# Kernel tuning notes

Hardware: AMD Instinct MI355X
Metric: run time of the kernel (lower is better)

## Reference

```python
import jax, jax.numpy as jnp
import numpy as np
from jax import lax

N_BLOCKS = 5
POOL = 15
N_HEADS = 8
LATENT = 32
N_EXPERTS = 4


def setup_inputs() -> dict:
    key = jax.random.key(0)
    ks = jax.random.split(key, 24)
    B, T, D = 4, 2048, 512
    H = 2 * D  # expert_dim
    s = 0.02
    f = lambda k, shp: (jax.random.normal(k, shp, jnp.float32) * s)
    return {
        'x': jax.random.normal(ks[0], (B, T, D), jnp.float32),
        # TemporalGating gate_proj
        'tg_w': f(ks[1], (D, N_BLOCKS)), 'tg_b': jnp.zeros((N_BLOCKS,), jnp.float32),
        # DualScaleFusion
        'mp_w': f(ks[2], (D, D)), 'mp_b': jnp.zeros((D,), jnp.float32),
        'fu_w': f(ks[3], (2 * D, D)), 'fu_b': jnp.zeros((D,), jnp.float32),
        # MLAAttention (all no-bias)
        'wc': f(ks[4], (D, LATENT)), 'wk': f(ks[5], (LATENT, D)),
        'wv': f(ks[6], (LATENT, D)), 'wq': f(ks[7], (D, D)), 'wo': f(ks[8], (D, D)),
        # RMSNorms
        's1': jnp.ones((D,), jnp.float32), 's2': jnp.ones((D,), jnp.float32),
        # GatedMoE
        'wr': f(ks[9], (D, N_EXPERTS)), 'br': jnp.zeros((N_EXPERTS,), jnp.float32),
        'wg': f(ks[10], (D, D)), 'bg': jnp.zeros((D,), jnp.float32),
        'w1': f(ks[11], (N_EXPERTS, D, H)), 'b1': jnp.zeros((N_EXPERTS, H), jnp.float32),
        'w2': f(ks[12], (N_EXPERTS, H, D)), 'b2': jnp.zeros((N_EXPERTS, D), jnp.float32),
    }


def _temporal_gate(x, tg_w, tg_b):
    B, T, D = x.shape
    bs = T // N_BLOCKS
    tl = N_BLOCKS * bs
    r = x[:, :tl].reshape(B, N_BLOCKS, bs, D)          # [B,nb,bs,D]
    bm = r.mean(axis=2)                                 # [B,nb,D]
    imp = jax.nn.softmax(bm @ tg_w + tg_b, axis=-1)     # [B,nb,nb]
    imp = imp.mean(axis=-1, keepdims=True)              # [B,nb,1]
    g = (r * imp[..., None]).reshape(B, tl, D)
    return jnp.pad(g, ((0, 0), (0, T - tl), (0, 0)))


def _dual_scale(x, mp_w, mp_b, fu_w, fu_b):
    # AveragePooling1D(pool=15, stride=1, SAME): TF excludes padding from the mean.
    B, T, D = x.shape
    sums = lax.reduce_window(x, 0.0, lax.add, (1, POOL, 1), (1, 1, 1), 'SAME')
    cnt = lax.reduce_window(jnp.ones((1, T, 1), x.dtype), 0.0, lax.add,
                            (1, POOL, 1), (1, 1, 1), 'SAME')
    macro = sums / cnt
    macro_feat = macro @ mp_w + mp_b
    return jnp.concatenate([x, macro_feat], axis=-1) @ fu_w + fu_b


def _mla_attn(x, wc, wk, wv, wq, wo):
    B, T, D = x.shape
    dh = D // N_HEADS
    split = lambda t: t.reshape(B, T, N_HEADS, dh).transpose(0, 2, 1, 3)
    latent = x @ wc                                      # [B,T,L]
    K, V, Q = split(latent @ wk), split(latent @ wv), split(x @ wq)
    scores = jnp.einsum('bhqd,bhkd->bhqk', Q, K) / jnp.sqrt(jnp.float32(dh))
    causal = jnp.tril(jnp.ones((T, T), jnp.float32))
    scores = scores + (1.0 - causal) * -1e9
    attn = jax.nn.softmax(scores, axis=-1)
    out = jnp.einsum('bhqk,bhkd->bhqd', attn, V).transpose(0, 2, 1, 3).reshape(B, T, D)
    return out @ wo


def _rmsnorm(x, scale, eps=1e-6):
    var = jnp.mean(jnp.square(x), axis=-1, keepdims=True)
    return scale * (x * lax.rsqrt(var + eps))


def _moe(x, wr, br, wg, bg, w1, b1, w2, b2):
    w = jax.nn.softmax(x @ wr + br, axis=-1)             # [B,T,E]
    xg = x * jax.nn.sigmoid(x @ wg + bg)
    h = jax.nn.gelu(jnp.einsum('btd,edh->bteh', xg, w1) + b1, approximate=False)
    eo = jnp.einsum('bteh,ehd->bted', h, w2) + b2        # [B,T,E,D]
    return jnp.einsum('bted,bte->btd', eo, w)


def reference(x, tg_w, tg_b, mp_w, mp_b, fu_w, fu_b, wc, wk, wv, wq, wo,
              s1, s2, wr, br, wg, bg, w1, b1, w2, b2):
    xf = _temporal_gate(x, tg_w, tg_b)
    xfu = _dual_scale(xf, mp_w, mp_b, fu_w, fu_b)
    x1 = _rmsnorm(x + _mla_attn(xfu, wc, wk, wv, wq, wo), s1)
    return _rmsnorm(x1 + _moe(x1, wr, br, wg, bg, w1, b1, w2, b2), s2)
```

## Files before the change

kernel.cpp:

```cpp
#include <hip/hip_runtime.h>
#include <math.h>

#define B_   4
#define T_   2048
#define D_   512
#define TOK  (B_*T_)
#define TL_  2045
#define GATE 0.2f

typedef unsigned short u16;
typedef __attribute__((ext_vector_type(8))) short short8;
typedef __attribute__((ext_vector_type(4))) float f32x4;

static __device__ __forceinline__ u16 f2u(float f){
    union { float f; unsigned u; } a; a.f = f;
    unsigned r = a.u + 0x7fffu + ((a.u >> 16) & 1u);
    return (u16)(r >> 16);
}
static __device__ __forceinline__ float u2f(u16 u){
    union { unsigned u; float f; } a; a.u = ((unsigned)u) << 16;
    return a.f;
}
static __device__ __forceinline__ f32x4 mfma16(short8 a, short8 b, f32x4 c){
    return __builtin_amdgcn_mfma_f32_16x16x32_bf16(a, b, c, 0, 0, 0);
}
static __device__ __forceinline__ void glds16(const u16* g, u16* l){
    __builtin_amdgcn_global_load_lds((const __attribute__((address_space(1))) void*)g,
                                     (__attribute__((address_space(3))) void*)l, 16, 0, 0);
}

__global__ __launch_bounds__(256) void gatepool_kernel(
    const float* __restrict__ x, u16* __restrict__ xfcat)
{
    int idx = blockIdx.x*256 + threadIdx.x;
    int d = idx & 511, g = idx >> 9;
    int b = g >> 7, t0 = (g & 127) << 4;
    const float* xp = x + ((size_t)b*2048)*512 + d;
    float v[30];
    #pragma unroll
    for (int j = 0; j < 30; ++j){
        int u = t0 - 7 + j;
        v[j] = (u >= 0 && u < TL_) ? xp[(size_t)u*512] : 0.f;
    }
    float p[31]; p[0] = 0.f;
    #pragma unroll
    for (int j = 0; j < 30; ++j) p[j+1] = p[j] + v[j];
    u16* xc = xfcat + ((size_t)(b*2048 + t0))*1024 + d;
    #pragma unroll
    for (int i = 0; i < 16; ++i){
        int t = t0 + i;
        float sum = p[i+15] - p[i];
        int lo = t-7; if (lo < 0) lo = 0;
        int hi = t+7; if (hi > 2047) hi = 2047;
        xc[(size_t)i*1024]       = f2u((t < TL_) ? GATE*v[i+7] : 0.f);
        xc[(size_t)i*1024 + 512] = f2u(GATE * sum / (float)(hi - lo + 1));
    }
}

struct TJob { const float* src; u16* dst; int K, N, ldout, coloff, tiles; float scale; };
struct TJobs { TJob j[12]; int n; };

__global__ __launch_bounds__(256) void tconv_all_kernel(TJobs JJ){
    __shared__ float t[32][33];
    int idx = blockIdx.x;
    int jb = 0;
    while (jb < JJ.n - 1 && idx >= JJ.j[jb].tiles){ idx -= JJ.j[jb].tiles; ++jb; }
    TJob J = JJ.j[jb];
    int tX = J.N >> 5;
    int k0 = (idx / tX) * 32, n0 = (idx % tX) * 32;
    int tx = threadIdx.x & 31, ty = threadIdx.x >> 5;
    #pragma unroll
    for (int i = 0; i < 32; i += 8)
        t[ty+i][tx] = J.src[(size_t)(k0+ty+i)*J.N + n0+tx];
    __syncthreads();
    #pragma unroll
    for (int i = 0; i < 32; i += 8)
        J.dst[(size_t)(n0+ty+i)*J.ldout + J.coloff + k0+tx] = f2u(J.scale * t[tx][ty+i]);
}

__global__ void convert_kernel(const float* __restrict__ in, u16* __restrict__ out){
    int idx = blockIdx.x*256 + threadIdx.x;
    out[idx] = f2u(in[idx]);
}

__global__ __launch_bounds__(256) void biasfold_kernel(
    const float* __restrict__ fu_b, const float* __restrict__ mp_b,
    const float* __restrict__ fu_w, float* __restrict__ out)
{
    int n = blockIdx.x, tid = threadIdx.x;
    float s = mp_b[tid]*fu_w[(size_t)(512+tid)*512 + n]
            + mp_b[tid+256]*fu_w[(size_t)(768+tid)*512 + n];
    for (int off = 32; off; off >>= 1) s += __shfl_down(s, off);
    __shared__ float ws[4];
    if ((tid & 63) == 0) ws[tid >> 6] = s;
    __syncthreads();
    if (tid == 0) out[n] = fu_b[n] + ws[0]+ws[1]+ws[2]+ws[3];
}

__global__ __launch_bounds__(256) void sgemm_kernel(const float* __restrict__ A,
    const float* __restrict__ B, u16* __restrict__ dstT, int ldT, int K){
    __shared__ float As[16][65];
    __shared__ float Bs[16][65];
    int tid = threadIdx.x;
    int tx = tid & 15, ty = tid >> 4;
    int m0 = blockIdx.y*64, n0 = blockIdx.x*64;
    int arow = tid >> 2, akq = (tid & 3) * 4;
    int bk = tid >> 4, bn = (tid & 15) * 4;
    float acc[4][4] = {};
    for (int k0 = 0; k0 < K; k0 += 16){
        const float* Ap = A + (size_t)(m0+arow)*K + k0 + akq;
        As[akq+0][arow]=Ap[0]; As[akq+1][arow]=Ap[1];
        As[akq+2][arow]=Ap[2]; As[akq+3][arow]=Ap[3];
        const float* Bp = B + (size_t)(k0+bk)*512 + n0 + bn;
        Bs[bk][bn+0]=Bp[0]; Bs[bk][bn+1]=Bp[1];
        Bs[bk][bn+2]=Bp[2]; Bs[bk][bn+3]=Bp[3];
        __syncthreads();
        #pragma unroll
        for (int kk = 0; kk < 16; ++kk){
            float av[4], bv[4];
            #pragma unroll
            for (int i=0;i<4;++i) av[i]=As[kk][ty*4+i];
            #pragma unroll
            for (int j=0;j<4;++j) bv[j]=Bs[kk][tx*4+j];
            #pragma unroll
            for (int i=0;i<4;++i)
                #pragma unroll
                for (int j=0;j<4;++j) acc[i][j] += av[i]*bv[j];
        }
        __syncthreads();
    }
    #pragma unroll
    for (int i=0;i<4;++i)
        #pragma unroll
        for (int j=0;j<4;++j)
            dstT[(size_t)(n0+tx*4+j)*ldT + m0+ty*4+i] = f2u(acc[i][j]);
}

#define GF_GELU   1
#define GF_ACCUM  2
#define GF_RSCOL  4
#define GF_GLU    8
#define GF_F32OUT 16
#define GF_TRANS  32

template<int MT>
__global__ __launch_bounds__(256) void mgemm_kernel(
    const u16* __restrict__ A, int lda, const u16* __restrict__ Bt, int ldb,
    const float* __restrict__ bias, const float* __restrict__ rs,
    const u16* __restrict__ glu, void* __restrict__ Cp, int ldc,
    int K, int flags)
{
    constexpr int MI = MT/32;
    __shared__ u16 As[MT*64];
    __shared__ u16 Bs[128*64];
    int tid = threadIdx.x;
    int wave = tid >> 6, lane = tid & 63;
    int n16 = lane & 15, quad = lane >> 4;
    int m0 = blockIdx.y * MT, n0 = blockIdx.x * 128;
    int wr = (wave >> 1) * (MT/2), wc = (wave & 1) * 64;

    f32x4 acc[MI][4] = {};

    for (int k0 = 0; k0 < K; k0 += 64){
        #pragma unroll
        for (int i = 0; i < MT/32; ++i){
            int s = i*256 + tid;
            int row = s >> 3, g = (s & 7) ^ (row & 7);
            glds16(A + (size_t)(m0+row)*lda + k0 + g*8, As + (size_t)s*8);
        }
        #pragma unroll
        for (int i = 0; i < 4; ++i){
            int s = i*256 + tid;
            int row = s >> 3, g = (s & 7) ^ (row & 7);
            glds16(Bt + (size_t)(n0+row)*ldb + k0 + g*8, Bs + (size_t)s*8);
        }
        __syncthreads();
        #pragma unroll
        for (int ks = 0; ks < 2; ++ks){
            short8 af[MI], bf[4];
            #pragma unroll
            for (int mi = 0; mi < MI; ++mi){
                int row = wr + mi*16 + n16;
                int g = (ks*4 + quad) ^ (row & 7);
                af[mi] = *(const short8*)&As[row*64 + g*8];
            }
            #pragma unroll
            for (int ni = 0; ni < 4; ++ni){
                int row = wc + ni*16 + n16;
                int g = (ks*4 + quad) ^ (row & 7);
                bf[ni] = *(const short8*)&Bs[row*64 + g*8];
            }
            #pragma unroll
            for (int mi = 0; mi < MI; ++mi)
                #pragma unroll
                for (int ni = 0; ni < 4; ++ni)
                    acc[mi][ni] = mfma16(af[mi], bf[ni], acc[mi][ni]);
        }
        __syncthreads();
    }

    if (flags & GF_TRANS){
        #pragma unroll
        for (int mi = 0; mi < MI; ++mi){
            int row0 = m0 + wr + mi*16 + quad*4;
            #pragma unroll
            for (int ni = 0; ni < 4; ++ni){
                int col = n0 + wc + ni*16 + n16;
                ushort4 h4;
                h4.x = f2u(acc[mi][ni][0]); h4.y = f2u(acc[mi][ni][1]);
                h4.z = f2u(acc[mi][ni][2]); h4.w = f2u(acc[mi][ni][3]);
                *(ushort4*)&((u16*)Cp)[(size_t)col*ldc + row0] = h4;
            }
        }
        return;
    }

    #pragma unroll
    for (int mi = 0; mi < MI; ++mi){
        #pragma unroll
        for (int reg = 0; reg < 4; ++reg){
            int row = m0 + wr + mi*16 + quad*4 + reg;
            #pragma unroll
            for (int ni = 0; ni < 4; ++ni){
                int col = n0 + wc + ni*16 + n16;
                float v = acc[mi][ni][reg];
                if (bias) v += bias[col];
                if (flags & GF_GELU)  v = 0.5f*v*(1.f + erff(v*0.70710678118f));
                if (flags & GF_GLU)   v = u2f(glu[(size_t)row*512 + col]) / (1.f + __expf(-v));
                if (flags & GF_RSCOL) v *= rs[(size_t)row*4 + (col >> 10)];
                size_t ci = (size_t)row*ldc + col;
                if (flags & GF_ACCUM)       ((float*)Cp)[ci] += v;
                else if (flags & GF_F32OUT) ((float*)Cp)[ci]  = v;
                else                        ((u16*)Cp)[ci]    = f2u(v);
            }
        }
    }
}

__global__ __launch_bounds__(256) void flash_kernel(
    const u16* __restrict__ QK,
    const u16* __restrict__ VT,
    u16* __restrict__ O)
{
    int bid = blockIdx.x;
    int qt = 15 - (bid >> 5);
    int bh = bid & 31;
    int h = bh & 7, b = bh >> 3;
    __shared__ u16 Ks[64*64];
    __shared__ u16 Vt[64*64];
    __shared__ u16 Ps[4][32*64];
    int tid = threadIdx.x;
    int wave = tid >> 6, lane = tid & 63;
    int n16 = lane & 15, quad = lane >> 4;
    size_t btok = (size_t)b*2048;
    size_t tok0 = btok + qt*128;
    int rowbase[2];
    rowbase[0] = qt*128 + wave*32;
    rowbase[1] = rowbase[0] + 16;

    short8 aq[2][2];
    #pragma unroll
    for (int mi = 0; mi < 2; ++mi)
        #pragma unroll
        for (int ks = 0; ks < 2; ++ks)
            aq[mi][ks] = *(const short8*)&QK[(tok0 + wave*32 + mi*16 + n16)*1024
                                            + h*64 + ks*32 + quad*8];

    float m_st[2][4], l_st[2][4];
    #pragma unroll
    for (int mi = 0; mi < 2; ++mi)
        #pragma unroll
        for (int r = 0; r < 4; ++r){ m_st[mi][r] = -3.0e38f; l_st[mi][r] = 0.f; }
    f32x4 ov[2][4] = {};

    int nkt = 2*qt + 2;
    for (int kt = 0; kt < nkt; ++kt){
        __syncthreads();
        {
            int r = tid >> 2;
            int g0 = (tid & 3) * 2;
            const uint4* kp = (const uint4*)&QK[(btok + kt*64 + r)*1024 + 512 + h*64 + g0*8];
            uint4 ka = kp[0], kb = kp[1];
            *(uint4*)&Ks[r*64 + ((g0  ) ^ (r&7))*8] = ka;
            *(uint4*)&Ks[r*64 + ((g0+1) ^ (r&7))*8] = kb;
            const uint4* vp = (const uint4*)&VT[(size_t)(h*64 + r)*8192 + btok + kt*64 + g0*8];
            uint4 va = vp[0], vb = vp[1];
            *(uint4*)&Vt[r*64 + ((g0  ) ^ (r&7))*8] = va;
            *(uint4*)&Vt[r*64 + ((g0+1) ^ (r&7))*8] = vb;
        }
        __syncthreads();

        #pragma unroll
        for (int mi = 0; mi < 2; ++mi){
            if (kt*64 > rowbase[mi] + 15) continue;
            f32x4 s[4];
            #pragma unroll
            for (int ct = 0; ct < 4; ++ct){
                f32x4 a = {};
                #pragma unroll
                for (int ks = 0; ks < 2; ++ks){
                    short8 bk = *(const short8*)&Ks[(ct*16+n16)*64 + (((ks*4+quad) ^ (n16&7))*8)];
                    a = mfma16(aq[mi][ks], bk, a);
                }
                s[ct] = a;
            }
            if (kt*64 + 63 > rowbase[mi]){
                #pragma unroll
                for (int ct = 0; ct < 4; ++ct){
                    int col = kt*64 + ct*16 + n16;
                    #pragma unroll
                    for (int r = 0; r < 4; ++r)
                        if (col > rowbase[mi] + quad*4 + r) s[ct][r] = -3.0e38f;
                }
            }
            #pragma unroll
            for (int r = 0; r < 4; ++r){
                float mx = fmaxf(fmaxf(s[0][r], s[1][r]), fmaxf(s[2][r], s[3][r]));
                #pragma unroll
                for (int off = 1; off < 16; off <<= 1) mx = fmaxf(mx, __shfl_xor(mx, off));
                float mn = fmaxf(m_st[mi][r], mx);
                float al = __expf(m_st[mi][r] - mn);
                m_st[mi][r] = mn;
                float sum = 0.f;
                #pragma unroll
                for (int ct = 0; ct < 4; ++ct){
                    float p = __expf(s[ct][r] - mn);
                    s[ct][r] = p; sum += p;
                }
                #pragma unroll
                for (int off = 1; off < 16; off <<= 1) sum += __shfl_xor(sum, off);
                l_st[mi][r] = l_st[mi][r]*al + sum;
                #pragma unroll
                for (int dt = 0; dt < 4; ++dt) ov[mi][dt][r] *= al;
            }
            #pragma unroll
            for (int ct = 0; ct < 4; ++ct){
                int gg = ct*2 + (n16 >> 3);
                #pragma unroll
                for (int r = 0; r < 4; ++r){
                    int row = mi*16 + quad*4 + r;
                    Ps[wave][row*64 + ((gg ^ (row&7))*8) + (n16 & 7)] = f2u(s[ct][r]);
                }
            }
        }
        #pragma unroll
        for (int mi = 0; mi < 2; ++mi){
            if (kt*64 > rowbase[mi] + 15) continue;
            short8 ap[2];
            #pragma unroll
            for (int ks = 0; ks < 2; ++ks){
                int row = mi*16 + n16;
                ap[ks] = *(const short8*)&Ps[wave][row*64 + (((ks*4+quad) ^ (n16&7))*8)];
            }
            #pragma unroll
            for (int dt = 0; dt < 4; ++dt)
                #pragma unroll
                for (int ks = 0; ks < 2; ++ks){
                    short8 bv = *(const short8*)&Vt[(dt*16+n16)*64 + (((ks*4+quad) ^ (n16&7))*8)];
                    ov[mi][dt] = mfma16(ap[ks], bv, ov[mi][dt]);
                }
        }
    }
    #pragma unroll
    for (int mi = 0; mi < 2; ++mi)
        #pragma unroll
        for (int r = 0; r < 4; ++r){
            float inv = 1.f / l_st[mi][r];
            size_t row = tok0 + wave*32 + mi*16 + quad*4 + r;
            #pragma unroll
            for (int dt = 0; dt < 4; ++dt)
                O[row*512 + h*64 + dt*16 + n16] = f2u(ov[mi][dt][r] * inv);
        }
}

__global__ __launch_bounds__(256) void rmsnorm_kernel(
    const float* __restrict__ x, const u16* __restrict__ y,
    const float* __restrict__ scale, u16* __restrict__ out)
{
    int tok = blockIdx.x, tid = threadIdx.x;
    size_t base = (size_t)tok * 512;
    float v0 = x[base+tid]     + u2f(y[base+tid]);
    float v1 = x[base+tid+256] + u2f(y[base+tid+256]);
    float ss = v0*v0 + v1*v1;
    for (int off = 32; off; off >>= 1) ss += __shfl_down(ss, off);
    __shared__ float ws[4];
    if ((tid & 63) == 0) ws[tid >> 6] = ss;
    __syncthreads();
    float rstd = rsqrtf((ws[0]+ws[1]+ws[2]+ws[3])*(1.f/512.f) + 1e-6f);
    out[base+tid]     = f2u(scale[tid]     * v0 * rstd);
    out[base+tid+256] = f2u(scale[tid+256] * v1 * rstd);
}

__global__ __launch_bounds__(256) void final_kernel(
    const u16* __restrict__ x1, const float* __restrict__ moe,
    const float* __restrict__ rout, const float* __restrict__ b2,
    const float* __restrict__ scale, float* __restrict__ out)
{
    int tok = blockIdx.x, tid = threadIdx.x;
    size_t base = (size_t)tok * 512;
    float r0 = rout[tok*4+0], r1 = rout[tok*4+1], r2 = rout[tok*4+2], r3 = rout[tok*4+3];
    float bb0 = r0*b2[tid]     + r1*b2[512+tid]     + r2*b2[1024+tid]     + r3*b2[1536+tid];
    float bb1 = r0*b2[tid+256] + r1*b2[768+tid]     + r2*b2[1280+tid]     + r3*b2[1792+tid];
    float v0 = u2f(x1[base+tid])     + moe[base+tid]     + bb0;
    float v1 = u2f(x1[base+tid+256]) + moe[base+tid+256] + bb1;
    float ss = v0*v0 + v1*v1;
    for (int off = 32; off; off >>= 1) ss += __shfl_down(ss, off);
    __shared__ float ws[4];
    if ((tid & 63) == 0) ws[tid >> 6] = ss;
    __syncthreads();
    float rstd = rsqrtf((ws[0]+ws[1]+ws[2]+ws[3])*(1.f/512.f) + 1e-6f);
    out[base+tid]     = scale[tid]     * v0 * rstd;
    out[base+tid+256] = scale[tid+256] * v1 * rstd;
}

__global__ __launch_bounds__(256) void router_kernel(
    const u16* __restrict__ x1, const float* __restrict__ wr,
    const float* __restrict__ br, float* __restrict__ rout)
{
    int wid = threadIdx.x >> 6, lane = threadIdx.x & 63;
    int tok = blockIdx.x*4 + wid;
    const u16* xp = x1 + (size_t)tok*512;
    float p0=0.f, p1=0.f, p2=0.f, p3=0.f;
    for (int d = lane; d < 512; d += 64){
        float xv = u2f(xp[d]);
        p0 += xv*wr[d*4+0]; p1 += xv*wr[d*4+1];
        p2 += xv*wr[d*4+2]; p3 += xv*wr[d*4+3];
    }
    for (int off = 32; off; off >>= 1){
        p0 += __shfl_down(p0,off); p1 += __shfl_down(p1,off);
        p2 += __shfl_down(p2,off); p3 += __shfl_down(p3,off);
    }
    if (lane == 0){
        p0 += br[0]; p1 += br[1]; p2 += br[2]; p3 += br[3];
        float mx = fmaxf(fmaxf(p0,p1), fmaxf(p2,p3));
        float e0=__expf(p0-mx), e1=__expf(p1-mx), e2=__expf(p2-mx), e3=__expf(p3-mx);
        float inv = 1.f/(e0+e1+e2+e3);
        rout[tok*4+0]=e0*inv; rout[tok*4+1]=e1*inv;
        rout[tok*4+2]=e2*inv; rout[tok*4+3]=e3*inv;
    }
}

extern "C" void kernel_launch(void* const* d_in, const int* in_sizes, int n_in,
                              void* d_out, int out_size, void* d_ws, size_t ws_size,
                              hipStream_t stream)
{
    const float* x    = (const float*)d_in[0];
    const float* mp_w = (const float*)d_in[3];
    const float* mp_b = (const float*)d_in[4];
    const float* fu_w = (const float*)d_in[5];
    const float* fu_b = (const float*)d_in[6];
    const float* wc   = (const float*)d_in[7];
    const float* wk   = (const float*)d_in[8];
    const float* wv   = (const float*)d_in[9];
    const float* wq   = (const float*)d_in[10];
    const float* wo   = (const float*)d_in[11];
    const float* s1   = (const float*)d_in[12];
    const float* s2   = (const float*)d_in[13];
    const float* wr   = (const float*)d_in[14];
    const float* br   = (const float*)d_in[15];
    const float* wg   = (const float*)d_in[16];
    const float* bg   = (const float*)d_in[17];
    const float* w1   = (const float*)d_in[18];
    const float* b1   = (const float*)d_in[19];
    const float* w2   = (const float*)d_in[20];
    const float* b2   = (const float*)d_in[21];

    char* wsb = (char*)d_ws;
    const size_t MB = 1024*1024;
    u16*   wqkT   = (u16*)(wsb + 0);
    u16*   wcvT   = (u16*)(wsb + 1*MB);
    u16*   woT    = (u16*)(wsb + (3*MB)/2);
    u16*   wgT    = (u16*)(wsb + 2*MB);
    u16*   WfuT2  = (u16*)(wsb + (5*MB)/2);
    u16*   fuBT   = (u16*)(wsb + (7*MB)/2);
    u16*   mp_wB  = (u16*)(wsb + 4*MB);
    u16*   w1T    = (u16*)(wsb + (9*MB)/2);
    u16*   w2Ts   = (u16*)(wsb + (17*MB)/2);
    float* fubias = (float*)(wsb + (25*MB)/2);
    float* ROUT   = (float*)(wsb + (25*MB)/2 + 4096);
    u16*   XFcat = (u16*)(wsb + 13*MB);
    float* MOE   = (float*)(wsb + 13*MB);
    u16*   S3    = (u16*)(wsb + 13*MB);
    u16*   XFU   = (u16*)(wsb + 29*MB);
    u16*   XG    = (u16*)(wsb + 29*MB);
    u16*   QKb   = (u16*)(wsb + 37*MB);
    u16*   Hb    = (u16*)(wsb + 37*MB);
    u16*   VbT   = (u16*)(wsb + 53*MB);
    u16*   ATT   = (u16*)(wsb + 61*MB);
    u16*   x1h   = (u16*)(wsb + 69*MB);

    auto mg128 = [&](const u16* A, int lda, const u16* Bt, int ldb, const float* bias,
                     const float* rs, const u16* glu, void* C, int ldc,
                     int M, int N, int K, int flags){
        dim3 g(N/128, M/128);
        mgemm_kernel<128><<<g, 256, 0, stream>>>(A, lda, Bt, ldb, bias, rs, glu, C, ldc, K, flags);
    };
    auto mg64 = [&](const u16* A, int lda, const u16* Bt, int ldb, const float* bias,
                    const float* rs, const u16* glu, void* C, int ldc,
                    int M, int N, int K, int flags){
        dim3 g(N/128, M/64);
        mgemm_kernel<64><<<g, 256, 0, stream>>>(A, lda, Bt, ldb, bias, rs, glu, C, ldc, K, flags);
    };

    TJobs JJ;
    auto setj = [&](int i, const float* src, u16* dst, int K, int N, int ldout,
                    int coloff, float scale){
        JJ.j[i] = TJob{src, dst, K, N, ldout, coloff, (K/32)*(N/32), scale};
    };
    setj(0, wq,            wqkT,  512,  512,  512, 0, 0.125f);
    setj(1, wo,            woT,   512,  512,  512, 0, 1.f);
    setj(2, wg,            wgT,   512,  512,  512, 0, 1.f);
    setj(3, fu_w,          WfuT2, 512,  512, 1024, 0, 1.f);
    setj(4, fu_w + 512*512,fuBT,  512,  512,  512, 0, 1.f);
    int nt = 5*256;
    for (int e = 0; e < 4; ++e){
        setj(5+e, w1 + (size_t)e*512*1024, w1T + (size_t)e*1024*512, 512, 1024, 512, 0, 1.f);
        nt += 512;
    }
    JJ.n = 12;
    setj(9,  w2,                      w2Ts, 1024, 512, 4096, 0,    1.f);
    setj(10, w2 + (size_t)1*1024*512, w2Ts, 1024, 512, 4096, 1024, 1.f);
    setj(11, w2 + (size_t)2*1024*512, w2Ts, 1024, 512, 4096, 2048, 1.f);
    nt += 3*512;
    tconv_all_kernel<<<nt, 256, 0, stream>>>(JJ);
    TJobs J2; J2.n = 1;
    J2.j[0] = TJob{w2 + (size_t)3*1024*512, w2Ts, 1024, 512, 4096, 3072, 512, 1.f};
    tconv_all_kernel<<<512, 256, 0, stream>>>(J2);
    convert_kernel<<<512*512/256, 256, 0, stream>>>(mp_w, mp_wB);
    sgemm_kernel<<<dim3(8,8), 256, 0, stream>>>(wc, wk, wqkT + 512*512, 512, 32);
    sgemm_kernel<<<dim3(8,8), 256, 0, stream>>>(wc, wv, wcvT, 512, 32);
    biasfold_kernel<<<512, 256, 0, stream>>>(fu_b, mp_b, fu_w, fubias);
    mg64(fuBT, 512, mp_wB, 512, 0, 0, 0, WfuT2 + 512, 1024, 512, 512, 512, 0);

    gatepool_kernel<<<(TOK/16)*512/256, 256, 0, stream>>>(x, XFcat);
    mg64 (XFcat, 1024, WfuT2, 1024, fubias, 0, 0, XFU, 512, TOK, 512, 1024, 0);
    mg128(XFU, 512, wqkT, 512, 0, 0, 0, QKb, 1024, TOK, 1024, 512, 0);
    mg64 (XFU, 512, wcvT, 512, 0, 0, 0, VbT, 8192, TOK, 512, 512, GF_TRANS);
    flash_kernel<<<512, 256, 0, stream>>>(QKb, VbT, ATT);
    mg64 (ATT, 512, woT, 512, 0, 0, 0, S3, 512, TOK, 512, 512, 0);
    rmsnorm_kernel<<<TOK, 256, 0, stream>>>(x, S3, s1, x1h);
    router_kernel<<<TOK/4, 256, 0, stream>>>(x1h, wr, br, ROUT);
    mg64 (x1h, 512, wgT, 512, bg, 0, x1h, XG, 512, TOK, 512, 512, GF_GLU);
    for (int p = 0; p < 2; ++p){
        mg128(XG, 512, w1T + (size_t)p*2048*512, 512, b1 + p*2048, ROUT + p*2, 0,
              Hb, 2048, TOK, 2048, 512, GF_GELU | GF_RSCOL);
        mg64 (Hb, 2048, w2Ts + p*2048, 4096, 0, 0, 0,
              MOE, 512, TOK, 512, 2048, p ? GF_ACCUM : GF_F32OUT);
    }
    final_kernel<<<TOK, 256, 0, stream>>>(x1h, MOE, ROUT, b2, s2, (float*)d_out);
}
```

Before: 631.3 us.

## Fuse QK and V projections into one GEMM and restructure flash softmax

```diff
diff --git a/kernel.cpp b/kernel.cpp
--- a/kernel.cpp
+++ b/kernel.cpp
@@ -7,6 +7,7 @@
 #define TOK  (B_*T_)
 #define TL_  2045
 #define GATE 0.2f
+#define QSCALE 0.18033688011112043f
 
 typedef unsigned short u16;
 typedef __attribute__((ext_vector_type(8))) short short8;
@@ -58,7 +59,7 @@
 }
 
 struct TJob { const float* src; u16* dst; int K, N, ldout, coloff, tiles; float scale; };
-struct TJobs { TJob j[12]; int n; };
+struct TJobs { TJob j[13]; int n; };
 
 __global__ __launch_bounds__(256) void tconv_all_kernel(TJobs JJ){
     __shared__ float t[32][33];
@@ -98,7 +99,7 @@
 }
 
 __global__ __launch_bounds__(256) void sgemm_kernel(const float* __restrict__ A,
-    const float* __restrict__ B, u16* __restrict__ dstT, int ldT, int K){
+    const float* __restrict__ B, u16* __restrict__ dstT, float* __restrict__ outF, int K){
     __shared__ float As[16][65];
     __shared__ float Bs[16][65];
     int tid = threadIdx.x;
@@ -129,11 +130,19 @@
         }
         __syncthreads();
     }
-    #pragma unroll
-    for (int i=0;i<4;++i)
-        #pragma unroll
-        for (int j=0;j<4;++j)
-            dstT[(size_t)(n0+tx*4+j)*ldT + m0+ty*4+i] = f2u(acc[i][j]);
+    if (outF){
+        #pragma unroll
+        for (int i=0;i<4;++i)
+            #pragma unroll
+            for (int j=0;j<4;++j)
+                outF[(size_t)(m0+ty*4+i)*512 + n0+tx*4+j] = acc[i][j];
+    } else {
+        #pragma unroll
+        for (int i=0;i<4;++i)
+            #pragma unroll
+            for (int j=0;j<4;++j)
+                dstT[(size_t)(n0+tx*4+j)*512 + m0+ty*4+i] = f2u(acc[i][j]);
+    }
 }
 
 #define GF_GELU   1
@@ -141,14 +150,14 @@
 #define GF_RSCOL  4
 #define GF_GLU    8
 #define GF_F32OUT 16
-#define GF_TRANS  32
+#define GF_QKV    32
 
 template<int MT>
 __global__ __launch_bounds__(256) void mgemm_kernel(
     const u16* __restrict__ A, int lda, const u16* __restrict__ Bt, int ldb,
     const float* __restrict__ bias, const float* __restrict__ rs,
     const u16* __restrict__ glu, void* __restrict__ Cp, int ldc,
-    int K, int flags)
+    u16* __restrict__ Cp2, int K, int flags)
 {
     constexpr int MI = MT/32;
     __shared__ u16 As[MT*64];
@@ -199,17 +208,17 @@
         __syncthreads();
     }
 
-    if (flags & GF_TRANS){
+    if ((flags & GF_QKV) && n0 >= 1024){
         #pragma unroll
         for (int mi = 0; mi < MI; ++mi){
             int row0 = m0 + wr + mi*16 + quad*4;
             #pragma unroll
             for (int ni = 0; ni < 4; ++ni){
-                int col = n0 + wc + ni*16 + n16;
+                int col = n0 + wc + ni*16 + n16 - 1024;
                 ushort4 h4;
                 h4.x = f2u(acc[mi][ni][0]); h4.y = f2u(acc[mi][ni][1]);
                 h4.z = f2u(acc[mi][ni][2]); h4.w = f2u(acc[mi][ni][3]);
-                *(ushort4*)&((u16*)Cp)[(size_t)col*ldc + row0] = h4;
+                *(ushort4*)&Cp2[(size_t)col*8192 + row0] = h4;
             }
         }
         return;
@@ -254,23 +263,18 @@
     int n16 = lane & 15, quad = lane >> 4;
     size_t btok = (size_t)b*2048;
     size_t tok0 = btok + qt*128;
-    int rowbase[2];
-    rowbase[0] = qt*128 + wave*32;
-    rowbase[1] = rowbase[0] + 16;
-
-    short8 aq[2][2];
-    #pragma unroll
-    for (int mi = 0; mi < 2; ++mi)
+
+    short8 qf[2][2];
+    #pragma unroll
+    for (int g = 0; g < 2; ++g)
         #pragma unroll
         for (int ks = 0; ks < 2; ++ks)
-            aq[mi][ks] = *(const short8*)&QK[(tok0 + wave*32 + mi*16 + n16)*1024
-                                            + h*64 + ks*32 + quad*8];
-
-    float m_st[2][4], l_st[2][4];
-    #pragma unroll
-    for (int mi = 0; mi < 2; ++mi)
-        #pragma unroll
-        for (int r = 0; r < 4; ++r){ m_st[mi][r] = -3.0e38f; l_st[mi][r] = 0.f; }
+            qf[g][ks] = *(const short8*)&QK[(tok0 + wave*32 + g*16 + n16)*1024
+                                           + h*64 + ks*32 + quad*8];
+
+    int qlo[2];  qlo[0] = qt*128 + wave*32; qlo[1] = qlo[0] + 16;
+    int qrow[2]; qrow[0] = qlo[0] + n16;    qrow[1] = qlo[1] + n16;
+    float m_st[2] = {-3.0e38f, -3.0e38f}, l_st[2] = {0.f, 0.f};
     f32x4 ov[2][4] = {};
 
     int nkt = 2*qt + 2;
@@ -290,86 +294,94 @@
         }
         __syncthreads();
 
-        #pragma unroll
-        for (int mi = 0; mi < 2; ++mi){
-            if (kt*64 > rowbase[mi] + 15) continue;
-            f32x4 s[4];
+        bool act[2];
+        #pragma unroll
+        for (int g = 0; g < 2; ++g){
+            act[g] = (kt*64 <= qlo[g] + 15);
+            if (!act[g]) continue;
+            f32x4 st[4];
             #pragma unroll
             for (int ct = 0; ct < 4; ++ct){
                 f32x4 a = {};
                 #pragma unroll
                 for (int ks = 0; ks < 2; ++ks){
-                    short8 bk = *(const short8*)&Ks[(ct*16+n16)*64 + (((ks*4+quad) ^ (n16&7))*8)];
-                    a = mfma16(aq[mi][ks], bk, a);
+                    short8 kf = *(const short8*)&Ks[(ct*16+n16)*64 + (((ks*4+quad) ^ (n16&7))*8)];
+                    a = mfma16(kf, qf[g][ks], a);
                 }
-                s[ct] = a;
-            }
-            if (kt*64 + 63 > rowbase[mi]){
+                st[ct] = a;
+            }
+            if (kt*64 + 63 > qlo[g]){
                 #pragma unroll
                 for (int ct = 0; ct < 4; ++ct){
-                    int col = kt*64 + ct*16 + n16;
+                    int kb0 = kt*64 + ct*16 + quad*4;
                     #pragma unroll
                     for (int r = 0; r < 4; ++r)
-                        if (col > rowbase[mi] + quad*4 + r) s[ct][r] = -3.0e38f;
+                        if (kb0 + r > qrow[g]) st[ct][r] = -3.0e38f;
                 }
             }
+            float mx = fmaxf(fmaxf(fmaxf(st[0][0],st[0][1]),fmaxf(st[0][2],st[0][3])),
+                       fmaxf(fmaxf(fmaxf(st[1][0],st[1][1]),fmaxf(st[1][2],st[1][3])),
+                       fmaxf(fmaxf(fmaxf(st[2][0],st[2][1]),fmaxf(st[2][2],st[2][3])),
+                             fmaxf(fmaxf(st[3][0],st[3][1]),fmaxf(st[3][2],st[3][3])))));
+            mx = fmaxf(mx, __shfl_xor(mx, 16));
+            mx = fmaxf(mx, __shfl_xor(mx, 32));
+            float mn = fmaxf(m_st[g], mx);
+            float al = exp2f(m_st[g] - mn);
+            m_st[g] = mn;
+            float sum = 0.f;
+            #pragma unroll
+            for (int ct = 0; ct < 4; ++ct)
+                #pragma unroll
+                for (int r = 0; r < 4; ++r){
+                    float p = exp2f(st[ct][r] - mn);
+                    st[ct][r] = p; sum += p;
+                }
+            sum += __shfl_xor(sum, 16);
+            sum += __shfl_xor(sum, 32);
+            l_st[g] = l_st[g]*al + sum;
+            int qr = g*16 + n16;
+            #pragma unroll
+            for (int ct = 0; ct < 4; ++ct){
+                ushort4 h4;
+                h4.x = f2u(st[ct][0]); h4.y = f2u(st[ct][1]);
+                h4.z = f2u(st[ct][2]); h4.w = f2u(st[ct][3]);
+                int goff = ct*2 + (quad >> 1);
+                *(ushort4*)&Ps[wave][qr*64 + ((goff ^ (qr&7))*8) + (quad&1)*4] = h4;
+            }
             #pragma unroll
             for (int r = 0; r < 4; ++r){
-                float mx = fmaxf(fmaxf(s[0][r], s[1][r]), fmaxf(s[2][r], s[3][r]));
-                #pragma unroll
-                for (int off = 1; off < 16; off <<= 1) mx = fmaxf(mx, __shfl_xor(mx, off));
-                float mn = fmaxf(m_st[mi][r], mx);
-                float al = __expf(m_st[mi][r] - mn);
-                m_st[mi][r] = mn;
-                float sum = 0.f;
-                #pragma unroll
-                for (int ct = 0; ct < 4; ++ct){
-                    float p = __expf(s[ct][r] - mn);
-                    s[ct][r] = p; sum += p;
-                }
-                #pragma unroll
-                for (int off = 1; off < 16; off <<= 1) sum += __shfl_xor(sum, off);
-                l_st[mi][r] = l_st[mi][r]*al + sum;
-                #pragma unroll
-                for (int dt = 0; dt < 4; ++dt) ov[mi][dt][r] *= al;
-            }
-            #pragma unroll
-            for (int ct = 0; ct < 4; ++ct){
-                int gg = ct*2 + (n16 >> 3);
-                #pragma unroll
-                for (int r = 0; r < 4; ++r){
-                    int row = mi*16 + quad*4 + r;
-                    Ps[wave][row*64 + ((gg ^ (row&7))*8) + (n16 & 7)] = f2u(s[ct][r]);
-                }
-            }
-        }
-        #pragma unroll
-        for (int mi = 0; mi < 2; ++mi){
-            if (kt*64 > rowbase[mi] + 15) continue;
+                float aa = __shfl(al, quad*4 + r);
+                #pragma unroll
+                for (int dt = 0; dt < 4; ++dt) ov[g][dt][r] *= aa;
+            }
+        }
+        #pragma unroll
+        for (int g = 0; g < 2; ++g){
+            if (!act[g]) continue;
             short8 ap[2];
-            #pragma unroll
-            for (int ks = 0; ks < 2; ++ks){
-                int row = mi*16 + n16;
-                ap[ks] = *(const short8*)&Ps[wave][row*64 + (((ks*4+quad) ^ (n16&7))*8)];
-            }
+            int row = g*16 + n16;
+            #pragma unroll
+            for (int ks = 0; ks < 2; ++ks)
+                ap[ks] = *(const short8*)&Ps[wave][row*64 + (((ks*4+quad) ^ (row&7))*8)];
             #pragma unroll
             for (int dt = 0; dt < 4; ++dt)
                 #pragma unroll
                 for (int ks = 0; ks < 2; ++ks){
                     short8 bv = *(const short8*)&Vt[(dt*16+n16)*64 + (((ks*4+quad) ^ (n16&7))*8)];
-                    ov[mi][dt] = mfma16(ap[ks], bv, ov[mi][dt]);
+                    ov[g][dt] = mfma16(ap[ks], bv, ov[g][dt]);
                 }
         }
     }
     #pragma unroll
-    for (int mi = 0; mi < 2; ++mi)
+    for (int g = 0; g < 2; ++g)
         #pragma unroll
         for (int r = 0; r < 4; ++r){
-            float inv = 1.f / l_st[mi][r];
-            size_t row = tok0 + wave*32 + mi*16 + quad*4 + r;
+            float li = __shfl(l_st[g], quad*4 + r);
+            float inv = 1.f / li;
+            size_t row = tok0 + wave*32 + g*16 + quad*4 + r;
             #pragma unroll
             for (int dt = 0; dt < 4; ++dt)
-                O[row*512 + h*64 + dt*16 + n16] = f2u(ov[mi][dt][r] * inv);
+                O[row*512 + h*64 + dt*16 + n16] = f2u(ov[g][dt][r] * inv);
         }
 }
 
@@ -467,85 +479,78 @@
 
     char* wsb = (char*)d_ws;
     const size_t MB = 1024*1024;
-    u16*   wqkT   = (u16*)(wsb + 0);
-    u16*   wcvT   = (u16*)(wsb + 1*MB);
-    u16*   woT    = (u16*)(wsb + (3*MB)/2);
-    u16*   wgT    = (u16*)(wsb + 2*MB);
-    u16*   WfuT2  = (u16*)(wsb + (5*MB)/2);
-    u16*   fuBT   = (u16*)(wsb + (7*MB)/2);
-    u16*   mp_wB  = (u16*)(wsb + 4*MB);
-    u16*   w1T    = (u16*)(wsb + (9*MB)/2);
-    u16*   w2Ts   = (u16*)(wsb + (17*MB)/2);
-    float* fubias = (float*)(wsb + (25*MB)/2);
-    float* ROUT   = (float*)(wsb + (25*MB)/2 + 4096);
-    u16*   XFcat = (u16*)(wsb + 13*MB);
-    float* MOE   = (float*)(wsb + 13*MB);
-    u16*   S3    = (u16*)(wsb + 13*MB);
-    u16*   XFU   = (u16*)(wsb + 29*MB);
-    u16*   XG    = (u16*)(wsb + 29*MB);
-    u16*   QKb   = (u16*)(wsb + 37*MB);
-    u16*   Hb    = (u16*)(wsb + 37*MB);
-    u16*   VbT   = (u16*)(wsb + 53*MB);
-    u16*   ATT   = (u16*)(wsb + 61*MB);
-    u16*   x1h   = (u16*)(wsb + 69*MB);
+    const size_t KB512 = 512*1024;
+    u16*   wqkvT  = (u16*)(wsb + 0);
+    u16*   woT    = (u16*)(wsb + 3*KB512);
+    u16*   wgT    = (u16*)(wsb + 4*KB512);
+    u16*   WfuT2  = (u16*)(wsb + 5*KB512);
+    u16*   fuBT   = (u16*)(wsb + 7*KB512);
+    u16*   mp_wB  = (u16*)(wsb + 8*KB512);
+    u16*   w1T    = (u16*)(wsb + 9*KB512);
+    u16*   w2Ts   = (u16*)(wsb + 17*KB512);
+    float* WcvF   = (float*)(wsb + 25*KB512);
+    float* fubias = (float*)(wsb + 27*KB512);
+    float* ROUT   = (float*)(wsb + 27*KB512 + 4096);
+    u16*   XFcat = (u16*)(wsb + 14*MB);
+    float* MOE   = (float*)(wsb + 14*MB);
+    u16*   S3    = (u16*)(wsb + 14*MB);
+    u16*   XFU   = (u16*)(wsb + 30*MB);
+    u16*   XG    = (u16*)(wsb + 30*MB);
+    u16*   QKb   = (u16*)(wsb + 38*MB);
+    u16*   Hb    = (u16*)(wsb + 38*MB);
+    u16*   ATT   = (u16*)(wsb + 54*MB);
+    u16*   VbT   = (u16*)(wsb + 70*MB);
+    u16*   x1h   = (u16*)(wsb + 78*MB);
 
     auto mg128 = [&](const u16* A, int lda, const u16* Bt, int ldb, const float* bias,
-                     const float* rs, const u16* glu, void* C, int ldc,
+                     const float* rs, const u16* glu, void* C, int ldc, u16* C2,
                      int M, int N, int K, int flags){
         dim3 g(N/128, M/128);
-        mgemm_kernel<128><<<g, 256, 0, stream>>>(A, lda, Bt, ldb, bias, rs, glu, C, ldc, K, flags);
+        mgemm_kernel<128><<<g, 256, 0, stream>>>(A, lda, Bt, ldb, bias, rs, glu, C, ldc, C2, K, flags);
     };
     auto mg64 = [&](const u16* A, int lda, const u16* Bt, int ldb, const float* bias,
-                    const float* rs, const u16* glu, void* C, int ldc,
+                    const float* rs, const u16* glu, void* C, int ldc, u16* C2,
                     int M, int N, int K, int flags){
         dim3 g(N/128, M/64);
-        mgemm_kernel<64><<<g, 256, 0, stream>>>(A, lda, Bt, ldb, bias, rs, glu, C, ldc, K, flags);
+        mgemm_kernel<64><<<g, 256, 0, stream>>>(A, lda, Bt, ldb, bias, rs, glu, C, ldc, C2, K, flags);
     };
 
-    TJobs JJ;
+    TJobs JJ; JJ.n = 13;
     auto setj = [&](int i, const float* src, u16* dst, int K, int N, int ldout,
                     int coloff, float scale){
         JJ.j[i] = TJob{src, dst, K, N, ldout, coloff, (K/32)*(N/32), scale};
     };
-    setj(0, wq,            wqkT,  512,  512,  512, 0, 0.125f);
+    setj(0, wq,            wqkvT, 512,  512,  512, 0, QSCALE);
     setj(1, wo,            woT,   512,  512,  512, 0, 1.f);
     setj(2, wg,            wgT,   512,  512,  512, 0, 1.f);
     setj(3, fu_w,          WfuT2, 512,  512, 1024, 0, 1.f);
     setj(4, fu_w + 512*512,fuBT,  512,  512,  512, 0, 1.f);
-    int nt = 5*256;
     for (int e = 0; e < 4; ++e){
         setj(5+e, w1 + (size_t)e*512*1024, w1T + (size_t)e*1024*512, 512, 1024, 512, 0, 1.f);
-        nt += 512;
-    }
-    JJ.n = 12;
-    setj(9,  w2,                      w2Ts, 1024, 512, 4096, 0,    1.f);
-    setj(10, w2 + (size_t)1*1024*512, w2Ts, 1024, 512, 4096, 1024, 1.f);
-    setj(11, w2 + (size_t)2*1024*512, w2Ts, 1024, 512, 4096, 2048, 1.f);
-    nt += 3*512;
+        setj(9+e, w2 + (size_t)e*1024*512, w2Ts + (size_t)e*1024, 1024, 512, 4096, 0, 1.f);
+    }
+    int nt = 5*256 + 4*512 + 4*512;
     tconv_all_kernel<<<nt, 256, 0, stream>>>(JJ);
-    TJobs J2; J2.n = 1;
-    J2.j[0] = TJob{w2 + (size_t)3*1024*512, w2Ts, 1024, 512, 4096, 3072, 512, 1.f};
-    tconv_all_kernel<<<512, 256, 0, stream>>>(J2);
     convert_kernel<<<512*512/256, 256, 0, stream>>>(mp_w, mp_wB);
-    sgemm_kernel<<<dim3(8,8), 256, 0, stream>>>(wc, wk, wqkT + 512*512, 512, 32);
-    sgemm_kernel<<<dim3(8,8), 256, 0, stream>>>(wc, wv, wcvT, 512, 32);
+    sgemm_kernel<<<dim3(8,8), 256, 0, stream>>>(wc, wk, wqkvT + 512*512, nullptr, 32);
+    sgemm_kernel<<<dim3(8,8), 256, 0, stream>>>(wc, wv, wqkvT + 1024*512, nullptr, 32);
     biasfold_kernel<<<512, 256, 0, stream>>>(fu_b, mp_b, fu_w, fubias);
-    mg64(fuBT, 512, mp_wB, 512, 0, 0, 0, WfuT2 + 512, 1024, 512, 512, 512, 0);
+    mg64(fuBT, 512, mp_wB, 512, 0, 0, 0, WfuT2 + 512, 1024, 0, 512, 512, 512, 0);
+    (void)WcvF;
 
     gatepool_kernel<<<(TOK/16)*512/256, 256, 0, stream>>>(x, XFcat);
-    mg64 (XFcat, 1024, WfuT2, 1024, fubias, 0, 0, XFU, 512, TOK, 512, 1024, 0);
-    mg128(XFU, 512, wqkT, 512, 0, 0, 0, QKb, 1024, TOK, 1024, 512, 0);
-    mg64 (XFU, 512, wcvT, 512, 0, 0, 0, VbT, 8192, TOK, 512, 512, GF_TRANS);
+    mg64 (XFcat, 1024, WfuT2, 1024, fubias, 0, 0, XFU, 512, 0, TOK, 512, 1024, 0);
+    mg64 (XFU, 512, wqkvT, 512, 0, 0, 0, QKb, 1024, VbT, TOK, 1536, 512, GF_QKV);
     flash_kernel<<<512, 256, 0, stream>>>(QKb, VbT, ATT);
-    mg64 (ATT, 512, woT, 512, 0, 0, 0, S3, 512, TOK, 512, 512, 0);
+    mg64 (ATT, 512, woT, 512, 0, 0, 0, S3, 512, 0, TOK, 512, 512, 0);
     rmsnorm_kernel<<<TOK, 256, 0, stream>>>(x, S3, s1, x1h);
     router_kernel<<<TOK/4, 256, 0, stream>>>(x1h, wr, br, ROUT);
-    mg64 (x1h, 512, wgT, 512, bg, 0, x1h, XG, 512, TOK, 512, 512, GF_GLU);
+    mg64 (x1h, 512, wgT, 512, bg, 0, x1h, XG, 512, 0, TOK, 512, 512, GF_GLU);
     for (int p = 0; p < 2; ++p){
         mg128(XG, 512, w1T + (size_t)p*2048*512, 512, b1 + p*2048, ROUT + p*2, 0,
-              Hb, 2048, TOK, 2048, 512, GF_GELU | GF_RSCOL);
+              Hb, 2048, 0, TOK, 2048, 512, GF_GELU | GF_RSCOL);
         mg64 (Hb, 2048, w2Ts + p*2048, 4096, 0, 0, 0,
-              MOE, 512, TOK, 512, 2048, p ? GF_ACCUM : GF_F32OUT);
+              MOE, 512, 0, TOK, 512, 2048, p ? GF_ACCUM : GF_F32OUT);
     }
     final_kernel<<<TOK, 256, 0, stream>>>(x1h, MOE, ROUT, b2, s2, (float*)d_out);
 }
```

Result: faster. 588.2 us (-6.8%).
